# Kernel tuning notes

Measured on AMD Instinct MI355X. Metric: run time of the kernel, lower is better.

The kernel has to match this reference:

```python
import math
import jax, jax.numpy as jnp
import numpy as np

R_MIN, R_MAX, R_BINS = 0.0, 10.0, 64
Z_MIN, Z_MAX, Z_BINS = -2.0, 2.0, 64
DR = (R_MAX - R_MIN) / R_BINS
DZ = (Z_MAX - Z_MIN) / Z_BINS
N = 16777216


def setup_inputs() -> dict:
    key = jax.random.key(0)
    k1, k2 = jax.random.split(key)
    positions = jax.random.normal(k1, (N, 3), dtype=jnp.float32)
    masses = jax.random.uniform(k2, (N,), dtype=jnp.float32)
    return {"positions": positions, "masses": masses}


def _volume():
    redge = R_MIN + jnp.arange(R_BINS + 1, dtype=jnp.float32) * DR
    area = math.pi * (redge[1:] ** 2 - redge[:-1] ** 2)  # [R_BINS]
    return area * DZ


def reference(positions, masses):
    r_cyl = jnp.sqrt(positions[:, 0] ** 2 + positions[:, 1] ** 2)
    i = jnp.floor((r_cyl - R_MIN) / DR).astype(jnp.int32)
    j = jnp.floor((positions[:, 2] - Z_MIN) / DZ).astype(jnp.int32)
    gd = (i >= 0) & (i < R_BINS) & (j >= 0) & (j < Z_BINS)
    flat = jnp.where(gd, i * Z_BINS + j, 0)
    w = jnp.where(gd, masses, 0.0)
    mass_in_bin = jnp.zeros((R_BINS * Z_BINS,), dtype=masses.dtype).at[flat].add(w)
    mass_in_bin = mass_in_bin.reshape(R_BINS, Z_BINS)
    surface_density = mass_in_bin / _volume()[:, None]
    return surface_density
```

## Files before the change

kernel.cpp:

```cpp
#include <hip/hip_runtime.h>
#include <math.h>

#define R_BINS 64
#define Z_BINS 64
#define NBINS (R_BINS * Z_BINS)

static constexpr float DR     = 10.0f / 64.0f;
static constexpr float DZ     = 4.0f  / 64.0f;
static constexpr float INV_DR = 64.0f / 10.0f;
static constexpr float INV_DZ = 16.0f;
static constexpr float ZMIN   = -2.0f;

__global__ __launch_bounds__(256) void hist_kernel(const float4* __restrict__ pos4,
                                                   const float4* __restrict__ mass4,
                                                   float* __restrict__ gbins,
                                                   int nquads) {
    __shared__ float lbins[NBINS];
    for (int b = threadIdx.x; b < NBINS; b += blockDim.x) lbins[b] = 0.0f;
    __syncthreads();

    const int stride = gridDim.x * blockDim.x;
    for (int q = blockIdx.x * blockDim.x + threadIdx.x; q < nquads; q += stride) {
        const float4 p0 = pos4[3 * q + 0];
        const float4 p1 = pos4[3 * q + 1];
        const float4 p2 = pos4[3 * q + 2];
        const float4 m  = mass4[q];

        const float xs[4] = {p0.x, p0.w, p1.z, p2.y};
        const float ys[4] = {p0.y, p1.x, p1.w, p2.z};
        const float zs[4] = {p0.z, p1.y, p2.x, p2.w};
        const float ms[4] = {m.x, m.y, m.z, m.w};

#pragma unroll
        for (int k = 0; k < 4; ++k) {
            const float r = sqrtf(xs[k] * xs[k] + ys[k] * ys[k]);
            const int i = (int)floorf(r * INV_DR);
            const int j = (int)floorf((zs[k] - ZMIN) * INV_DZ);
            if (i < R_BINS && (unsigned)j < (unsigned)Z_BINS) {
                atomicAdd(&lbins[i * Z_BINS + j], ms[k]);
            }
        }
    }

    __syncthreads();
    for (int b = threadIdx.x; b < NBINS; b += blockDim.x) {
        const float v = lbins[b];
        if (v != 0.0f) atomicAdd(&gbins[b], v);
    }
}

__global__ __launch_bounds__(256) void finalize_kernel(const float* __restrict__ gbins,
                                                       float* __restrict__ out) {
    const int idx = blockIdx.x * blockDim.x + threadIdx.x;
    if (idx < NBINS) {
        const int i = idx / Z_BINS;
        const float r0 = (float)i * DR;
        const float r1 = (float)(i + 1) * DR;
        const float area = (float)M_PI * (r1 * r1 - r0 * r0);
        out[idx] = gbins[idx] / (area * DZ);
    }
}

extern "C" void kernel_launch(void* const* d_in, const int* in_sizes, int n_in,
                              void* d_out, int out_size, void* d_ws, size_t ws_size,
                              hipStream_t stream) {
    const float* positions = (const float*)d_in[0];
    const float* masses    = (const float*)d_in[1];
    float* out   = (float*)d_out;
    float* gbins = (float*)d_ws;

    const int n = in_sizes[1];
    const int nquads = n / 4;

    hipMemsetAsync(gbins, 0, NBINS * sizeof(float), stream);

    const int block = 256;
    const int grid  = 1024;
    hist_kernel<<<grid, block, 0, stream>>>((const float4*)positions,
                                            (const float4*)masses,
                                            gbins, nquads);

    finalize_kernel<<<(NBINS + block - 1) / block, block, 0, stream>>>(gbins, out);
}
```

Baseline: 331.5 us.

## Stage per-wave position chunks through LDS for coalesced loads, use 512-thread blocks

Each wave now loads a contiguous 256-particle chunk of positions with fully coalesced float4 loads, stages it in shared memory, then reads x/y/z per particle from LDS. Masses are loaded as coalesced scalars instead of float4. This replaces the strided float4 access pattern, where each thread read 48 contiguous bytes, and raises the block size to 512. It adds LDS traffic and wave-level barriers, plus a tail kernel for leftover particles. The floor on the radius is replaced by truncation, which is safe because the radius is non-negative.

```diff
diff --git a/kernel.cpp b/kernel.cpp
--- a/kernel.cpp
+++ b/kernel.cpp
@@ -4,48 +4,87 @@
 #define R_BINS 64
 #define Z_BINS 64
 #define NBINS (R_BINS * Z_BINS)
+#define BLOCK 512
+#define WAVES_PER_BLOCK 8
+#define GRID 1024
 
 static constexpr float DR     = 10.0f / 64.0f;
 static constexpr float DZ     = 4.0f  / 64.0f;
-static constexpr float INV_DR = 64.0f / 10.0f;
+static constexpr float INV_DR = 6.4f;
 static constexpr float INV_DZ = 16.0f;
-static constexpr float ZMIN   = -2.0f;
 
-__global__ __launch_bounds__(256) void hist_kernel(const float4* __restrict__ pos4,
-                                                   const float4* __restrict__ mass4,
-                                                   float* __restrict__ gbins,
-                                                   int nquads) {
+__global__ __launch_bounds__(BLOCK) void hist_kernel(const float4* __restrict__ pos4,
+                                                     const float* __restrict__ mass,
+                                                     float* __restrict__ gbins,
+                                                     int nchunks) {
     __shared__ float lbins[NBINS];
-    for (int b = threadIdx.x; b < NBINS; b += blockDim.x) lbins[b] = 0.0f;
+    __shared__ float4 stage[WAVES_PER_BLOCK][192];
+
+    const int lane = threadIdx.x & 63;
+    const int w    = threadIdx.x >> 6;
+
+    for (int b = threadIdx.x; b < NBINS; b += BLOCK) lbins[b] = 0.0f;
     __syncthreads();
 
-    const int stride = gridDim.x * blockDim.x;
-    for (int q = blockIdx.x * blockDim.x + threadIdx.x; q < nquads; q += stride) {
-        const float4 p0 = pos4[3 * q + 0];
-        const float4 p1 = pos4[3 * q + 1];
-        const float4 p2 = pos4[3 * q + 2];
-        const float4 m  = mass4[q];
+    const int totalWaves = gridDim.x * WAVES_PER_BLOCK;
+    float* s = (float*)&stage[w][0];
 
-        const float xs[4] = {p0.x, p0.w, p1.z, p2.y};
-        const float ys[4] = {p0.y, p1.x, p1.w, p2.z};
-        const float zs[4] = {p0.z, p1.y, p2.x, p2.w};
-        const float ms[4] = {m.x, m.y, m.z, m.w};
+    for (int c = blockIdx.x * WAVES_PER_BLOCK + w; c < nchunks; c += totalWaves) {
+        const float4* pb = pos4 + (size_t)192 * c;
+        const float4 f0 = pb[lane];
+        const float4 f1 = pb[64 + lane];
+        const float4 f2 = pb[128 + lane];
 
+        const float* mb = mass + (size_t)256 * c;
+        const float m0 = mb[lane];
+        const float m1 = mb[64 + lane];
+        const float m2 = mb[128 + lane];
+        const float m3 = mb[192 + lane];
+
+        stage[w][lane]       = f0;
+        stage[w][64 + lane]  = f1;
+        stage[w][128 + lane] = f2;
+        __asm__ volatile("s_waitcnt lgkmcnt(0)" ::: "memory");
+        __builtin_amdgcn_wave_barrier();
+
+        const float ms[4] = {m0, m1, m2, m3};
 #pragma unroll
         for (int k = 0; k < 4; ++k) {
-            const float r = sqrtf(xs[k] * xs[k] + ys[k] * ys[k]);
-            const int i = (int)floorf(r * INV_DR);
-            const int j = (int)floorf((zs[k] - ZMIN) * INV_DZ);
+            const int p = 64 * k + lane;
+            const float x = s[3 * p];
+            const float y = s[3 * p + 1];
+            const float z = s[3 * p + 2];
+            const float r = sqrtf(x * x + y * y);
+            const int i = (int)(r * INV_DR);
+            const int j = (int)floorf((z + 2.0f) * INV_DZ);
             if (i < R_BINS && (unsigned)j < (unsigned)Z_BINS) {
                 atomicAdd(&lbins[i * Z_BINS + j], ms[k]);
             }
         }
+        __asm__ volatile("" ::: "memory");
+        __builtin_amdgcn_wave_barrier();
     }
 
     __syncthreads();
-    for (int b = threadIdx.x; b < NBINS; b += blockDim.x) {
+    for (int b = threadIdx.x; b < NBINS; b += BLOCK) {
         const float v = lbins[b];
         if (v != 0.0f) atomicAdd(&gbins[b], v);
+    }
+}
+
+__global__ void tail_kernel(const float* __restrict__ pos,
+                            const float* __restrict__ mass,
+                            float* __restrict__ gbins,
+                            int start, int n) {
+    const int t = start + blockIdx.x * blockDim.x + threadIdx.x;
+    if (t < n) {
+        const float x = pos[3 * t], y = pos[3 * t + 1], z = pos[3 * t + 2];
+        const float r = sqrtf(x * x + y * y);
+        const int i = (int)(r * INV_DR);
+        const int j = (int)floorf((z + 2.0f) * INV_DZ);
+        if (i < R_BINS && (unsigned)j < (unsigned)Z_BINS) {
+            atomicAdd(&gbins[i * Z_BINS + j], mass[t]);
+        }
     }
 }
 
@@ -70,15 +109,16 @@
     float* gbins = (float*)d_ws;
 
     const int n = in_sizes[1];
-    const int nquads = n / 4;
+    const int nchunks = n / 256;
+    const int rem = n - nchunks * 256;
 
     hipMemsetAsync(gbins, 0, NBINS * sizeof(float), stream);
 
-    const int block = 256;
-    const int grid  = 1024;
-    hist_kernel<<<grid, block, 0, stream>>>((const float4*)positions,
-                                            (const float4*)masses,
-                                            gbins, nquads);
-
-    finalize_kernel<<<(NBINS + block - 1) / block, block, 0, stream>>>(gbins, out);
+    hist_kernel<<<GRID, BLOCK, 0, stream>>>((const float4*)positions, masses,
+                                            gbins, nchunks);
+    if (rem > 0) {
+        tail_kernel<<<(rem + 255) / 256, 256, 0, stream>>>(positions, masses,
+                                                           gbins, nchunks * 256, n);
+    }
+    finalize_kernel<<<(NBINS + 255) / 256, 256, 0, stream>>>(gbins, out);
 }
```

Result: no change. 327.6 us (-1.2%).
